# Kernel optimization log

Hardware: AMD Instinct MI355X
Metric: run time of the kernel (lower is better)

## Reference

```python
import jax, jax.numpy as jnp
import numpy as np

# dims (match init_kwargs)
B, S, HID = 2, 2048, 2048
NH = 16
DN = 128   # qk_nope_head_dim
DR = 64    # qk_rope_head_dim
DV = 128   # v_head_dim
QLR = 1536 # q_lora_rank
KVLR = 512 # kv_lora_rank
QHD = DN + DR  # 192
ROPE_BASE = 10000.0
EPS = 1e-6


def rms_norm(x, w):
    # ZeroCenteredRMSNorm: weight is zero-centered, scale = (1 + w)
    var = jnp.mean(x * x, axis=-1, keepdims=True)
    return x * jax.lax.rsqrt(var + EPS) * (1.0 + w)


def rotate_half(x):
    d = x.shape[-1] // 2
    return jnp.concatenate([-x[..., d:], x[..., :d]], axis=-1)


def deinterleave(x):
    # rearrange '(d_pairs two) -> (two d_pairs)'
    return jnp.concatenate([x[..., 0::2], x[..., 1::2]], axis=-1)


def setup_inputs() -> dict:
    key = jax.random.key(0)
    ks = jax.random.split(key, 8)
    s = 0.02
    return {
        "hidden_states": jax.random.normal(ks[0], (B, S, HID), jnp.float32),
        "position_ids": jnp.arange(S, dtype=jnp.int32),
        "Wq_down": jax.random.normal(ks[1], (HID, QLR), jnp.float32) * s,
        "q_norm_w": jnp.zeros((QLR,), jnp.float32),
        "Wq_up": jax.random.normal(ks[2], (QLR, NH * QHD), jnp.float32) * s,
        "Wkv_down": jax.random.normal(ks[3], (HID, KVLR + DR), jnp.float32) * s,
        "kv_norm_w": jnp.zeros((KVLR,), jnp.float32),
        "Wkv_up": jax.random.normal(ks[4], (KVLR, NH * (DN + DV)), jnp.float32) * s,
        "W_gate": jax.random.normal(ks[5], (HID, NH * DV), jnp.float32) * s,
        "W_out": jax.random.normal(ks[6], (NH * DV, HID), jnp.float32) * s,
    }


def reference(hidden_states, position_ids, Wq_down, q_norm_w, Wq_up,
              Wkv_down, kv_norm_w, Wkv_up, W_gate, W_out):
    bsz, q_len, _ = hidden_states.shape
    pos = jnp.broadcast_to(position_ids[None, :], (bsz, q_len))  # [b,s]

    # Q path: down-proj -> RMSNorm -> up-proj -> [b,h,s,QHD]
    q = rms_norm(hidden_states @ Wq_down, q_norm_w) @ Wq_up
    q = q.reshape(bsz, q_len, NH, QHD).transpose(0, 2, 1, 3)
    q_nope, q_rope = q[..., :DN], q[..., DN:]

    # KV path: joint down-proj -> split latent / rope key
    ckv = hidden_states @ Wkv_down                     # [b,s,KVLR+DR]
    c_kv, k_rope = ckv[..., :KVLR], ckv[..., KVLR:]
    k_rope = k_rope[:, None, :, :]                     # [b,1,s,DR]
    kv = rms_norm(c_kv, kv_norm_w) @ Wkv_up            # [b,s,NH*(DN+DV)]
    kv = kv.reshape(bsz, q_len, NH, DN + DV).transpose(0, 2, 1, 3)
    k_nope, v = kv[..., :DN], kv[..., DN:]

    # partial RoPE on rope dims (with the '(pairs two)->(two pairs)' permute)
    inv_freq = 1.0 / (ROPE_BASE ** (jnp.arange(0, DR, 2, dtype=jnp.float32) / DR))
    freqs = pos[..., None].astype(jnp.float32) * inv_freq  # [b,s,DR/2]
    emb = jnp.concatenate([freqs, freqs], axis=-1)          # [b,s,DR]
    cos = jnp.cos(emb)[:, None, :, :]                       # [b,1,s,DR]
    sin = jnp.sin(emb)[:, None, :, :]
    q_r = deinterleave(q_rope)
    k_r = deinterleave(k_rope)
    q_r = q_r * cos + rotate_half(q_r) * sin
    k_r = k_r * cos + rotate_half(k_r) * sin

    query = jnp.concatenate([q_nope, q_r], axis=-1)                       # [b,h,s,QHD]
    key = jnp.concatenate([k_nope, jnp.broadcast_to(k_r, k_nope.shape[:-1] + (DR,))], axis=-1)

    scores = jnp.einsum('bhqd,bhkd->bhqk', query, key) / np.sqrt(QHD)
    attn = jax.nn.softmax(scores, axis=-1)
    out = jnp.einsum('bhqk,bhkd->bhqd', attn, v)                          # [b,h,s,DV]
    out = out.transpose(0, 2, 1, 3)                                       # [b,s,h,DV]

    gate = jax.nn.sigmoid(hidden_states @ W_gate).reshape(bsz, q_len, NH, DV)
    out = (out * gate).reshape(bsz, q_len, NH * DV)
    return out @ W_out
```

## Files before the change

kernel.cpp:

```cpp
#include <hip/hip_runtime.h>
#include <math.h>

#define BT 2
#define SL 2048
#define HIDN 2048
#define NHEADS 16
#define DNOPE 128
#define DROPE 64
#define DVAL 128
#define QHEAD 192
#define QLRANK 1536
#define KVLRANK 512
#define TTOK (BT * SL)

typedef unsigned short u16;
typedef u16 u16x4 __attribute__((ext_vector_type(4)));
typedef u16 u16x8 __attribute__((ext_vector_type(8)));
typedef short bf16x8 __attribute__((ext_vector_type(8)));
typedef float f32x4 __attribute__((ext_vector_type(4)));

__device__ __forceinline__ u16 f2b(float f) {
    union { float f; unsigned u; } v; v.f = f;
    unsigned r = v.u + 0x7FFFu + ((v.u >> 16) & 1u);
    return (u16)(r >> 16);
}
__device__ __forceinline__ float b2f(u16 h) {
    union { unsigned u; float f; } v; v.u = ((unsigned)h) << 16;
    return v.f;
}

__device__ __forceinline__ void gl2lds16(const u16* g, u16* l) {
    __builtin_amdgcn_global_load_lds((const __attribute__((address_space(1))) unsigned int*)g,
                                     (__attribute__((address_space(3))) unsigned int*)l, 16, 0, 0);
}

__global__ __launch_bounds__(256) void cast_k(const float* __restrict__ in, u16* __restrict__ out,
                                              int n4) {
    int i = blockIdx.x * 256 + threadIdx.x;
    const int stride = gridDim.x * 256;
    for (; i < n4; i += stride) {
        const float4 v = ((const float4*)in)[i];
        u16x4 u;
        u.x = f2b(v.x); u.y = f2b(v.y); u.z = f2b(v.z); u.w = f2b(v.w);
        ((u16x4*)out)[i] = u;
    }
}

__global__ __launch_bounds__(256) void tcast_k(const float* __restrict__ in, u16* __restrict__ out,
                                               int R, int C) {
    __shared__ u16 tile[64][72];
    const int c0 = blockIdx.x * 64, r0 = blockIdx.y * 64;
    const int t = threadIdx.x;
    const int tr = t >> 4, tc4 = (t & 15) * 4;
#pragma unroll
    for (int i = 0; i < 4; ++i) {
        const int r = tr + i * 16;
        const float4 v = *(const float4*)&in[(r0 + r) * C + c0 + tc4];
        u16x4 u;
        u.x = f2b(v.x); u.y = f2b(v.y); u.z = f2b(v.z); u.w = f2b(v.w);
        *(u16x4*)&tile[r][tc4] = u;
    }
    __syncthreads();
#pragma unroll
    for (int i = 0; i < 4; ++i) {
        const int rr = tr + i * 16;
        u16x4 u;
        u.x = tile[tc4 + 0][rr];
        u.y = tile[tc4 + 1][rr];
        u.z = tile[tc4 + 2][rr];
        u.w = tile[tc4 + 3][rr];
        *(u16x4*)&out[(c0 + rr) * R + r0 + tc4] = u;
    }
}

__global__ __launch_bounds__(256) void vtrans_k(const u16* __restrict__ kvbuf,
                                                u16* __restrict__ vT) {
    __shared__ u16 tile[64][72];
    const int bh = blockIdx.z;
    const int b = bh >> 4, h = bh & 15;
    const int s0 = blockIdx.x * 64, d0 = blockIdx.y * 64;
    const int t = threadIdx.x;
    const int tr = t >> 4, tc4 = (t & 15) * 4;
#pragma unroll
    for (int i = 0; i < 4; ++i) {
        const int s = tr + i * 16;
        *(u16x4*)&tile[s][tc4] =
            *(const u16x4*)&kvbuf[(b * SL + s0 + s) * 4096 + h * 256 + 128 + d0 + tc4];
    }
    __syncthreads();
#pragma unroll
    for (int i = 0; i < 4; ++i) {
        const int dd = tr + i * 16;
        u16x4 u;
        u.x = tile[tc4 + 0][dd];
        u.y = tile[tc4 + 1][dd];
        u.z = tile[tc4 + 2][dd];
        u.w = tile[tc4 + 3][dd];
        *(u16x4*)&vT[(bh * 128 + d0 + dd) * SL + s0 + tc4] = u;
    }
}

template <int EPI, int OUTF>
__global__ __launch_bounds__(256) void gemm_bf16_k(const u16* __restrict__ A,
                                                   const u16* __restrict__ Bt,
                                                   void* __restrict__ Cv, int M, int N, int K) {
    __shared__ u16 As[128 * 64];
    __shared__ u16 Bs[128 * 64];
    const int t = threadIdx.x;
    const int nx = gridDim.x;
    const int bid = blockIdx.x + nx * blockIdx.y;
    const int cpx = (nx * gridDim.y) >> 3;
    const int swz = (bid & 7) * cpx + (bid >> 3);
    const int bn = (swz % nx) * 128, bm = (swz / nx) * 128;
    const int w = t >> 6, lane = t & 63;
    const int wr = (w >> 1) * 64, wc = (w & 1) * 64;
    const int lr = lane & 15, lg = lane >> 4;

    const int srow = w * 32 + (lane >> 3);
    const int scol = ((lane & 7) ^ ((lane >> 3) & 7)) * 8;
    const u16* Ag = A + (size_t)(bm + srow) * K + scol;
    const u16* Bg = Bt + (size_t)(bn + srow) * K + scol;
    u16* Asl = As + w * 2048;
    u16* Bsl = Bs + w * 2048;

    f32x4 acc[4][4];
#pragma unroll
    for (int i = 0; i < 4; ++i)
#pragma unroll
        for (int j = 0; j < 4; ++j) acc[i][j] = 0.f;

    for (int k0 = 0; k0 < K; k0 += 64) {
        __syncthreads();
#pragma unroll
        for (int j = 0; j < 4; ++j) gl2lds16(Ag + (size_t)(j * 8) * K + k0, Asl + j * 512);
#pragma unroll
        for (int j = 0; j < 4; ++j) gl2lds16(Bg + (size_t)(j * 8) * K + k0, Bsl + j * 512);
        __syncthreads();
#pragma unroll
        for (int kk = 0; kk < 2; ++kk) {
            bf16x8 af[4], bfr[4];
#pragma unroll
            for (int mi = 0; mi < 4; ++mi) {
                const int row = wr + mi * 16 + lr;
                const int idx = (row * 64 + kk * 32 + lg * 8) ^ ((row & 7) << 3);
                af[mi] = *(const bf16x8*)&As[idx];
            }
#pragma unroll
            for (int ni = 0; ni < 4; ++ni) {
                const int row = wc + ni * 16 + lr;
                const int idx = (row * 64 + kk * 32 + lg * 8) ^ ((row & 7) << 3);
                bfr[ni] = *(const bf16x8*)&Bs[idx];
            }
#pragma unroll
            for (int mi = 0; mi < 4; ++mi)
#pragma unroll
                for (int ni = 0; ni < 4; ++ni)
                    acc[mi][ni] = __builtin_amdgcn_mfma_f32_16x16x32_bf16(af[mi], bfr[ni],
                                                                          acc[mi][ni], 0, 0, 0);
        }
    }
#pragma unroll
    for (int mi = 0; mi < 4; ++mi)
#pragma unroll
        for (int ni = 0; ni < 4; ++ni)
#pragma unroll
            for (int r = 0; r < 4; ++r) {
                const int row = bm + wr + mi * 16 + lg * 4 + r;
                const int col = bn + wc + ni * 16 + lr;
                float v = acc[mi][ni][r];
                if (EPI == 1) v = 1.f / (1.f + __expf(-v));
                if (col < N) {
                    if (OUTF)
                        ((float*)Cv)[(size_t)row * N + col] = v;
                    else
                        ((u16*)Cv)[(size_t)row * N + col] = f2b(v);
                }
            }
}

__global__ __launch_bounds__(256) void rmsnorm_k(const u16* __restrict__ in, u16* __restrict__ out,
                                                 const float* __restrict__ w, int is, int os,
                                                 int n) {
    const int row = blockIdx.x;
    const int t = threadIdx.x;
    const u16* x = in + row * is;
    u16* y = out + row * os;
    float ss = 0.f;
    for (int d = t * 4; d < n; d += 1024) {
        const u16x4 u = *(const u16x4*)&x[d];
        const float a = b2f(u.x), b = b2f(u.y), c = b2f(u.z), e = b2f(u.w);
        ss += a * a + b * b + c * c + e * e;
    }
    ss += __shfl_down(ss, 32);
    ss += __shfl_down(ss, 16);
    ss += __shfl_down(ss, 8);
    ss += __shfl_down(ss, 4);
    ss += __shfl_down(ss, 2);
    ss += __shfl_down(ss, 1);
    __shared__ float red[5];
    if ((t & 63) == 0) red[t >> 6] = ss;
    __syncthreads();
    if (t == 0) red[4] = rsqrtf((red[0] + red[1] + red[2] + red[3]) / (float)n + 1e-6f);
    __syncthreads();
    const float sc = red[4];
    for (int d = t * 4; d < n; d += 1024) {
        const u16x4 u = *(const u16x4*)&x[d];
        const float4 wv = *(const float4*)&w[d];
        u16x4 o;
        o.x = f2b(b2f(u.x) * sc * (1.f + wv.x));
        o.y = f2b(b2f(u.y) * sc * (1.f + wv.y));
        o.z = f2b(b2f(u.z) * sc * (1.f + wv.z));
        o.w = f2b(b2f(u.w) * sc * (1.f + wv.w));
        *(u16x4*)&y[d] = o;
    }
}

__global__ __launch_bounds__(64) void rope_k(u16* __restrict__ q, const u16* __restrict__ ckv,
                                             u16* __restrict__ kr, const int* __restrict__ pos_ids) {
    const int tok = blockIdx.x * 2 + (threadIdx.x >> 5);
    const int j = threadIdx.x & 31;
    const int s = tok & (SL - 1);
    const float pos = (float)pos_ids[s];
    const float inv = 1.f / powf(10000.f, (float)(2 * j) / 64.f);
    const float f = pos * inv;
    const float c = cosf(f), sn = sinf(f);
    const u16* kc = ckv + tok * 576 + 512;
    const unsigned kp = *(const unsigned*)&kc[2 * j];
    const float ke = b2f((u16)(kp & 0xffff)), ko = b2f((u16)(kp >> 16));
    kr[tok * 64 + j] = f2b(ke * c - ko * sn);
    kr[tok * 64 + 32 + j] = f2b(ko * c + ke * sn);
#pragma unroll
    for (int h = 0; h < NHEADS; ++h) {
        u16* qb = q + tok * (NHEADS * QHEAD) + h * QHEAD + DNOPE;
        const unsigned qp = *(const unsigned*)&qb[2 * j];
        const float qe = b2f((u16)(qp & 0xffff)), qo = b2f((u16)(qp >> 16));
        qb[j] = f2b(qe * c - qo * sn);
        qb[32 + j] = f2b(qo * c + qe * sn);
    }
}

#define PSTR 76
__global__ __launch_bounds__(256, 2) void mla_attn_k(const u16* __restrict__ qbuf,
                                                     const u16* __restrict__ kvbuf,
                                                     const u16* __restrict__ kr,
                                                     const u16* __restrict__ vT,
                                                     const u16* __restrict__ gateb,
                                                     u16* __restrict__ outg) {
    __shared__ u16 Ks[64 * 200];
    __shared__ u16 Vt[128 * 72];
    __shared__ u16 Ps[4 * 32 * PSTR];
    const int bh = blockIdx.x;
    const int b = bh >> 4, h = bh & 15;
    const int q0 = blockIdx.y * 128;
    const int t = threadIdx.x, w = t >> 6, lane = t & 63;
    const int lr = lane & 15, lg = lane >> 4;
    const float scale = 0.07216878364870322f;

    int kRow[6], kC8[6];
#pragma unroll
    for (int c = 0; c < 6; ++c) {
        const int i = t + c * 256;
        kRow[c] = i / 24;
        kC8[c] = (i % 24) * 8;
    }
    int vRow[4], vC8[4];
#pragma unroll
    for (int c = 0; c < 4; ++c) {
        const int i = t + c * 256;
        vRow[c] = i >> 3;
        vC8[c] = (i & 7) * 8;
    }

    bf16x8 aq[2][6];
#pragma unroll
    for (int mi = 0; mi < 2; ++mi) {
        const int qrow = b * SL + q0 + w * 32 + mi * 16 + lr;
#pragma unroll
        for (int ks = 0; ks < 6; ++ks)
            aq[mi][ks] =
                *(const bf16x8*)&qbuf[(size_t)qrow * (NHEADS * QHEAD) + h * QHEAD + ks * 32 + lg * 8];
    }

    f32x4 O[2][8];
#pragma unroll
    for (int mi = 0; mi < 2; ++mi)
#pragma unroll
        for (int df = 0; df < 8; ++df) O[mi][df] = 0.f;
    float m[2][4], l[2][4];
#pragma unroll
    for (int mi = 0; mi < 2; ++mi)
#pragma unroll
        for (int r = 0; r < 4; ++r) {
            m[mi][r] = -INFINITY;
            l[mi][r] = 0.f;
        }

    u16x8 kreg[6], vreg[4];
#define ATTN_ISSUE_K(K0)                                                                     \
    {                                                                                        \
        _Pragma("unroll") for (int c = 0; c < 6; ++c) {                                      \
            const int tok = b * SL + (K0) + kRow[c];                                         \
            kreg[c] = (kC8[c] < 128)                                                         \
                          ? *(const u16x8*)&kvbuf[(size_t)tok * 4096 + h * 256 + kC8[c]]     \
                          : *(const u16x8*)&kr[(size_t)tok * 64 + (kC8[c] - 128)];           \
        }                                                                                    \
    }
#define ATTN_ISSUE_V(K0)                                                                     \
    {                                                                                        \
        _Pragma("unroll") for (int c = 0; c < 4; ++c)                                        \
            vreg[c] = *(const u16x8*)&vT[(size_t)(bh * 128 + vRow[c]) * SL + (K0) + vC8[c]]; \
    }

    ATTN_ISSUE_K(0);
    ATTN_ISSUE_V(0);

    for (int it = 0; it < SL / 64; ++it) {
        __syncthreads();
#pragma unroll
        for (int c = 0; c < 6; ++c) *(u16x8*)&Ks[kRow[c] * 200 + kC8[c]] = kreg[c];
#pragma unroll
        for (int c = 0; c < 4; ++c) *(u16x8*)&Vt[vRow[c] * 72 + vC8[c]] = vreg[c];
        __syncthreads();
        const bool more = (it + 1) < SL / 64;
        const int kn = (it + 1) * 64;
        if (more) ATTN_ISSUE_K(kn);

        f32x4 s[2][4];
#pragma unroll
        for (int mi = 0; mi < 2; ++mi)
#pragma unroll
            for (int nf = 0; nf < 4; ++nf) s[mi][nf] = 0.f;
#pragma unroll
        for (int ks = 0; ks < 6; ++ks) {
#pragma unroll
            for (int nf = 0; nf < 4; ++nf) {
                const bf16x8 bk = *(const bf16x8*)&Ks[(nf * 16 + lr) * 200 + ks * 32 + lg * 8];
                s[0][nf] = __builtin_amdgcn_mfma_f32_16x16x32_bf16(aq[0][ks], bk, s[0][nf], 0, 0, 0);
                s[1][nf] = __builtin_amdgcn_mfma_f32_16x16x32_bf16(aq[1][ks], bk, s[1][nf], 0, 0, 0);
            }
        }

        float lmv[2][4];
        float growth = -INFINITY;
#pragma unroll
        for (int mi = 0; mi < 2; ++mi)
#pragma unroll
            for (int r = 0; r < 4; ++r) {
                float lm = fmaxf(fmaxf(s[mi][0][r], s[mi][1][r]), fmaxf(s[mi][2][r], s[mi][3][r])) * scale;
                lm = fmaxf(lm, __shfl_xor(lm, 1));
                lm = fmaxf(lm, __shfl_xor(lm, 2));
                lm = fmaxf(lm, __shfl_xor(lm, 4));
                lm = fmaxf(lm, __shfl_xor(lm, 8));
                lmv[mi][r] = lm;
                growth = fmaxf(growth, lm - m[mi][r]);
            }
        const bool skip = __all(growth <= 8.f);

#pragma unroll
        for (int mi = 0; mi < 2; ++mi) {
            const int pb = w * 32 * PSTR + mi * 16 * PSTR;
#pragma unroll
            for (int r = 0; r < 4; ++r) {
                const float mn = skip ? m[mi][r] : fmaxf(m[mi][r], lmv[mi][r]);
                float p0 = __expf(s[mi][0][r] * scale - mn);
                float p1 = __expf(s[mi][1][r] * scale - mn);
                float p2 = __expf(s[mi][2][r] * scale - mn);
                float p3 = __expf(s[mi][3][r] * scale - mn);
                float ps = (p0 + p1) + (p2 + p3);
                ps += __shfl_xor(ps, 1);
                ps += __shfl_xor(ps, 2);
                ps += __shfl_xor(ps, 4);
                ps += __shfl_xor(ps, 8);
                if (skip) {
                    l[mi][r] += ps;
                } else {
                    const float al = __expf(m[mi][r] - mn);
                    l[mi][r] = l[mi][r] * al + ps;
                    m[mi][r] = mn;
#pragma unroll
                    for (int df = 0; df < 8; ++df) O[mi][df][r] *= al;
                }
                const int prow = pb + (lg * 4 + r) * PSTR + lr;
                Ps[prow] = f2b(p0);
                Ps[prow + 16] = f2b(p1);
                Ps[prow + 32] = f2b(p2);
                Ps[prow + 48] = f2b(p3);
            }
        }

        if (more) ATTN_ISSUE_V(kn);

        bf16x8 pa[2][2];
#pragma unroll
        for (int mi = 0; mi < 2; ++mi)
#pragma unroll
            for (int ks2 = 0; ks2 < 2; ++ks2)
                pa[mi][ks2] =
                    *(const bf16x8*)&Ps[w * 32 * PSTR + (mi * 16 + lr) * PSTR + ks2 * 32 + lg * 8];
#pragma unroll
        for (int df = 0; df < 8; ++df)
#pragma unroll
            for (int ks2 = 0; ks2 < 2; ++ks2) {
                const bf16x8 bv = *(const bf16x8*)&Vt[(df * 16 + lr) * 72 + ks2 * 32 + lg * 8];
                O[0][df] = __builtin_amdgcn_mfma_f32_16x16x32_bf16(pa[0][ks2], bv, O[0][df], 0, 0, 0);
                O[1][df] = __builtin_amdgcn_mfma_f32_16x16x32_bf16(pa[1][ks2], bv, O[1][df], 0, 0, 0);
            }
    }
#pragma unroll
    for (int mi = 0; mi < 2; ++mi) {
        float invl[4];
#pragma unroll
        for (int r = 0; r < 4; ++r) invl[r] = 1.f / l[mi][r];
#pragma unroll
        for (int df = 0; df < 8; ++df)
#pragma unroll
            for (int r = 0; r < 4; ++r) {
                const int qq = b * SL + q0 + w * 32 + mi * 16 + lg * 4 + r;
                const int col = h * DVAL + df * 16 + lr;
                const float o = O[mi][df][r] * invl[r];
                const float g = b2f(gateb[qq * (NHEADS * DVAL) + col]);
                outg[qq * (NHEADS * DVAL) + col] = f2b(o * g);
            }
    }
}

extern "C" void kernel_launch(void* const* d_in, const int* in_sizes, int n_in, void* d_out,
                              int out_size, void* d_ws, size_t ws_size, hipStream_t stream) {
    const float* hs = (const float*)d_in[0];
    const int* pos = (const int*)d_in[1];
    const float* Wq_down = (const float*)d_in[2];
    const float* q_norm_w = (const float*)d_in[3];
    const float* Wq_up = (const float*)d_in[4];
    const float* Wkv_down = (const float*)d_in[5];
    const float* kv_norm_w = (const float*)d_in[6];
    const float* Wkv_up = (const float*)d_in[7];
    const float* W_gate = (const float*)d_in[8];
    const float* W_out = (const float*)d_in[9];
    float* out = (float*)d_out;

    u16* p = (u16*)d_ws;
    u16* hs16 = p;      p += (size_t)TTOK * HIDN;
    u16* wqd_t = p;     p += (size_t)QLRANK * HIDN;
    u16* wqu_t = p;     p += (size_t)(NHEADS * QHEAD) * QLRANK;
    u16* wkvd_t = p;    p += (size_t)576 * HIDN;
    u16* wkvu_t = p;    p += (size_t)(NHEADS * 256) * KVLRANK;
    u16* wg_t = p;      p += (size_t)HIDN * HIDN;
    u16* wo_t = p;      p += (size_t)HIDN * (NHEADS * DVAL);
    u16* qdown = p;     p += (size_t)TTOK * QLRANK;
    u16* qbuf = p;      p += (size_t)TTOK * (NHEADS * QHEAD);
    u16* ckv = p;       p += (size_t)TTOK * 576;
    u16* kvn = p;       p += (size_t)TTOK * KVLRANK;
    u16* kvbuf = p;     p += (size_t)TTOK * (NHEADS * 256);
    u16* krb = p;       p += (size_t)TTOK * DROPE;
    u16* vTg = p;       p += (size_t)32 * 128 * SL;
    u16* gateb = p;     p += (size_t)TTOK * (NHEADS * DVAL);
    u16* outg = p;      p += (size_t)TTOK * (NHEADS * DVAL);

    const dim3 blk(256);

    cast_k<<<dim3(2048), blk, 0, stream>>>(hs, hs16, TTOK * HIDN / 4);
    tcast_k<<<dim3(QLRANK / 64, HIDN / 64), blk, 0, stream>>>(Wq_down, wqd_t, HIDN, QLRANK);
    tcast_k<<<dim3((NHEADS * QHEAD) / 64, QLRANK / 64), blk, 0, stream>>>(Wq_up, wqu_t, QLRANK,
                                                                          NHEADS * QHEAD);
    tcast_k<<<dim3(576 / 64, HIDN / 64), blk, 0, stream>>>(Wkv_down, wkvd_t, HIDN, 576);
    tcast_k<<<dim3((NHEADS * 256) / 64, KVLRANK / 64), blk, 0, stream>>>(Wkv_up, wkvu_t, KVLRANK,
                                                                         NHEADS * 256);
    tcast_k<<<dim3(HIDN / 64, HIDN / 64), blk, 0, stream>>>(W_gate, wg_t, HIDN, HIDN);
    tcast_k<<<dim3(HIDN / 64, (NHEADS * DVAL) / 64), blk, 0, stream>>>(W_out, wo_t, NHEADS * DVAL,
                                                                       HIDN);

    gemm_bf16_k<0, 0><<<dim3(QLRANK / 128, TTOK / 128), blk, 0, stream>>>(hs16, wqd_t, qdown, TTOK,
                                                                          QLRANK, HIDN);
    rmsnorm_k<<<dim3(TTOK), blk, 0, stream>>>(qdown, qdown, q_norm_w, QLRANK, QLRANK, QLRANK);
    gemm_bf16_k<0, 0><<<dim3((NHEADS * QHEAD) / 128, TTOK / 128), blk, 0, stream>>>(
        qdown, wqu_t, qbuf, TTOK, NHEADS * QHEAD, QLRANK);
    gemm_bf16_k<0, 0><<<dim3((576 + 127) / 128, TTOK / 128), blk, 0, stream>>>(hs16, wkvd_t, ckv,
                                                                               TTOK, 576, HIDN);
    rmsnorm_k<<<dim3(TTOK), blk, 0, stream>>>(ckv, kvn, kv_norm_w, 576, KVLRANK, KVLRANK);
    gemm_bf16_k<0, 0><<<dim3((NHEADS * 256) / 128, TTOK / 128), blk, 0, stream>>>(
        kvn, wkvu_t, kvbuf, TTOK, NHEADS * 256, KVLRANK);
    rope_k<<<dim3(TTOK / 2), dim3(64), 0, stream>>>(qbuf, ckv, krb, pos);
    vtrans_k<<<dim3(SL / 64, 2, 32), blk, 0, stream>>>(kvbuf, vTg);
    gemm_bf16_k<1, 0><<<dim3((NHEADS * DVAL) / 128, TTOK / 128), blk, 0, stream>>>(
        hs16, wg_t, gateb, TTOK, NHEADS * DVAL, HIDN);

    mla_attn_k<<<dim3(32, SL / 128), blk, 0, stream>>>(qbuf, kvbuf, krb, vTg, gateb, outg);

    gemm_bf16_k<0, 1><<<dim3(HIDN / 128, TTOK / 128), blk, 0, stream>>>(outg, wo_t, out, TTOK, HIDN,
                                                                        NHEADS * DVAL);
}
```

Measured before the change: 497.8 us.

## Fuse q-down, kv-down and gate projections into one wide GEMM

The three GEMMs that all read the bf16 hidden states (q down-projection, kv down-projection and the gate projection) become a single GEMM. It uses a concatenated transposed weight of width 4224 and applies the sigmoid epilogue only to the gate columns. The six weight transpose-cast launches are merged into one kernel, and the two RMSNorm launches into one. RoPE and attention now read their slices of the fused output buffer. This removes repeated reads of the activations, several kernel launches and the poorly-filled 576-wide GEMM. In exchange it computes 64 unused padding columns and uses a wider strided output layout.

```diff
diff --git a/kernel.cpp b/kernel.cpp
--- a/kernel.cpp
+++ b/kernel.cpp
@@ -12,6 +12,10 @@
 #define QLRANK 1536
 #define KVLRANK 512
 #define TTOK (BT * SL)
+#define FN 4224
+#define FC_CKV 1536
+#define FC_ROPE 2048
+#define FC_GATE 2176
 
 typedef unsigned short u16;
 typedef u16 u16x4 __attribute__((ext_vector_type(4)));
@@ -46,16 +50,15 @@
     }
 }
 
-__global__ __launch_bounds__(256) void tcast_k(const float* __restrict__ in, u16* __restrict__ out,
-                                               int R, int C) {
+__device__ __forceinline__ void tcast_tile(const float* __restrict__ in, u16* __restrict__ out,
+                                           int R, int C, int tx, int ty, int t) {
     __shared__ u16 tile[64][72];
-    const int c0 = blockIdx.x * 64, r0 = blockIdx.y * 64;
-    const int t = threadIdx.x;
+    const int c0 = tx * 64, r0 = ty * 64;
     const int tr = t >> 4, tc4 = (t & 15) * 4;
 #pragma unroll
     for (int i = 0; i < 4; ++i) {
         const int r = tr + i * 16;
-        const float4 v = *(const float4*)&in[(r0 + r) * C + c0 + tc4];
+        const float4 v = *(const float4*)&in[(size_t)(r0 + r) * C + c0 + tc4];
         u16x4 u;
         u.x = f2b(v.x); u.y = f2b(v.y); u.z = f2b(v.z); u.w = f2b(v.w);
         *(u16x4*)&tile[r][tc4] = u;
@@ -69,7 +72,35 @@
         u.y = tile[tc4 + 1][rr];
         u.z = tile[tc4 + 2][rr];
         u.w = tile[tc4 + 3][rr];
-        *(u16x4*)&out[(c0 + rr) * R + r0 + tc4] = u;
+        *(u16x4*)&out[(size_t)(c0 + rr) * R + r0 + tc4] = u;
+    }
+}
+
+__global__ __launch_bounds__(256) void tcast_all_k(
+    const float* __restrict__ Wq_down, const float* __restrict__ Wq_up,
+    const float* __restrict__ Wkv_down, const float* __restrict__ Wkv_up,
+    const float* __restrict__ W_gate, const float* __restrict__ W_out, u16* __restrict__ wqd_t,
+    u16* __restrict__ wqu_t, u16* __restrict__ wkvd_t, u16* __restrict__ wkvu_t,
+    u16* __restrict__ wg_t, u16* __restrict__ wo_t) {
+    const int tid = blockIdx.x;
+    const int t = threadIdx.x;
+    if (tid < 768) {
+        tcast_tile(Wq_down, wqd_t, 2048, 1536, tid % 24, tid / 24, t);
+    } else if (tid < 1920) {
+        const int i = tid - 768;
+        tcast_tile(Wq_up, wqu_t, 1536, 3072, i % 48, i / 48, t);
+    } else if (tid < 2208) {
+        const int i = tid - 1920;
+        tcast_tile(Wkv_down, wkvd_t, 2048, 576, i % 9, i / 9, t);
+    } else if (tid < 2720) {
+        const int i = tid - 2208;
+        tcast_tile(Wkv_up, wkvu_t, 512, 4096, i % 64, i / 64, t);
+    } else if (tid < 3744) {
+        const int i = tid - 2720;
+        tcast_tile(W_gate, wg_t, 2048, 2048, i % 32, i / 32, t);
+    } else {
+        const int i = tid - 3744;
+        tcast_tile(W_out, wo_t, 2048, 2048, i % 32, i / 32, t);
     }
 }
 
@@ -85,7 +116,7 @@
     for (int i = 0; i < 4; ++i) {
         const int s = tr + i * 16;
         *(u16x4*)&tile[s][tc4] =
-            *(const u16x4*)&kvbuf[(b * SL + s0 + s) * 4096 + h * 256 + 128 + d0 + tc4];
+            *(const u16x4*)&kvbuf[(size_t)(b * SL + s0 + s) * 4096 + h * 256 + 128 + d0 + tc4];
     }
     __syncthreads();
 #pragma unroll
@@ -96,7 +127,7 @@
         u.y = tile[tc4 + 1][dd];
         u.z = tile[tc4 + 2][dd];
         u.w = tile[tc4 + 3][dd];
-        *(u16x4*)&vT[(bh * 128 + d0 + dd) * SL + s0 + tc4] = u;
+        *(u16x4*)&vT[(size_t)(bh * 128 + d0 + dd) * SL + s0 + tc4] = u;
     }
 }
 
@@ -169,6 +200,7 @@
                 const int col = bn + wc + ni * 16 + lr;
                 float v = acc[mi][ni][r];
                 if (EPI == 1) v = 1.f / (1.f + __expf(-v));
+                if (EPI == 2 && col >= FC_GATE) v = 1.f / (1.f + __expf(-v));
                 if (col < N) {
                     if (OUTF)
                         ((float*)Cv)[(size_t)row * N + col] = v;
@@ -178,13 +210,18 @@
             }
 }
 
-__global__ __launch_bounds__(256) void rmsnorm_k(const u16* __restrict__ in, u16* __restrict__ out,
-                                                 const float* __restrict__ w, int is, int os,
-                                                 int n) {
-    const int row = blockIdx.x;
+__global__ __launch_bounds__(256) void rms2_k(const u16* __restrict__ fout,
+                                              const float* __restrict__ qw,
+                                              const float* __restrict__ kw, u16* __restrict__ qn,
+                                              u16* __restrict__ kvn) {
+    const int rid = blockIdx.x;
+    const bool isq = rid < TTOK;
+    const int row = isq ? rid : rid - TTOK;
+    const int n = isq ? QLRANK : KVLRANK;
+    const u16* x = fout + (size_t)row * FN + (isq ? 0 : FC_CKV);
+    const float* w = isq ? qw : kw;
+    u16* y = isq ? (qn + (size_t)row * QLRANK) : (kvn + (size_t)row * KVLRANK);
     const int t = threadIdx.x;
-    const u16* x = in + row * is;
-    u16* y = out + row * os;
     float ss = 0.f;
     for (int d = t * 4; d < n; d += 1024) {
         const u16x4 u = *(const u16x4*)&x[d];
@@ -215,7 +252,7 @@
     }
 }
 
-__global__ __launch_bounds__(64) void rope_k(u16* __restrict__ q, const u16* __restrict__ ckv,
+__global__ __launch_bounds__(64) void rope_k(u16* __restrict__ q, const u16* __restrict__ fout,
                                              u16* __restrict__ kr, const int* __restrict__ pos_ids) {
     const int tok = blockIdx.x * 2 + (threadIdx.x >> 5);
     const int j = threadIdx.x & 31;
@@ -224,14 +261,14 @@
     const float inv = 1.f / powf(10000.f, (float)(2 * j) / 64.f);
     const float f = pos * inv;
     const float c = cosf(f), sn = sinf(f);
-    const u16* kc = ckv + tok * 576 + 512;
+    const u16* kc = fout + (size_t)tok * FN + FC_ROPE;
     const unsigned kp = *(const unsigned*)&kc[2 * j];
     const float ke = b2f((u16)(kp & 0xffff)), ko = b2f((u16)(kp >> 16));
     kr[tok * 64 + j] = f2b(ke * c - ko * sn);
     kr[tok * 64 + 32 + j] = f2b(ko * c + ke * sn);
 #pragma unroll
     for (int h = 0; h < NHEADS; ++h) {
-        u16* qb = q + tok * (NHEADS * QHEAD) + h * QHEAD + DNOPE;
+        u16* qb = q + (size_t)tok * (NHEADS * QHEAD) + h * QHEAD + DNOPE;
         const unsigned qp = *(const unsigned*)&qb[2 * j];
         const float qe = b2f((u16)(qp & 0xffff)), qo = b2f((u16)(qp >> 16));
         qb[j] = f2b(qe * c - qo * sn);
@@ -418,8 +455,8 @@
                 const int qq = b * SL + q0 + w * 32 + mi * 16 + lg * 4 + r;
                 const int col = h * DVAL + df * 16 + lr;
                 const float o = O[mi][df][r] * invl[r];
-                const float g = b2f(gateb[qq * (NHEADS * DVAL) + col]);
-                outg[qq * (NHEADS * DVAL) + col] = f2b(o * g);
+                const float g = b2f(gateb[(size_t)qq * FN + col]);
+                outg[(size_t)qq * (NHEADS * DVAL) + col] = f2b(o * g);
             }
     }
 }
@@ -440,51 +477,39 @@
 
     u16* p = (u16*)d_ws;
     u16* hs16 = p;      p += (size_t)TTOK * HIDN;
-    u16* wqd_t = p;     p += (size_t)QLRANK * HIDN;
+    u16* wdown_t = p;   p += (size_t)FN * HIDN;
+    u16* wqd_t = wdown_t;
+    u16* wkvd_t = wdown_t + (size_t)QLRANK * HIDN;
+    u16* wg_t = wdown_t + (size_t)FC_GATE * HIDN;
     u16* wqu_t = p;     p += (size_t)(NHEADS * QHEAD) * QLRANK;
-    u16* wkvd_t = p;    p += (size_t)576 * HIDN;
     u16* wkvu_t = p;    p += (size_t)(NHEADS * 256) * KVLRANK;
-    u16* wg_t = p;      p += (size_t)HIDN * HIDN;
     u16* wo_t = p;      p += (size_t)HIDN * (NHEADS * DVAL);
-    u16* qdown = p;     p += (size_t)TTOK * QLRANK;
+    u16* fout = p;      p += (size_t)TTOK * FN;
+    u16* qdownN = p;    p += (size_t)TTOK * QLRANK;
     u16* qbuf = p;      p += (size_t)TTOK * (NHEADS * QHEAD);
-    u16* ckv = p;       p += (size_t)TTOK * 576;
     u16* kvn = p;       p += (size_t)TTOK * KVLRANK;
     u16* kvbuf = p;     p += (size_t)TTOK * (NHEADS * 256);
     u16* krb = p;       p += (size_t)TTOK * DROPE;
     u16* vTg = p;       p += (size_t)32 * 128 * SL;
-    u16* gateb = p;     p += (size_t)TTOK * (NHEADS * DVAL);
     u16* outg = p;      p += (size_t)TTOK * (NHEADS * DVAL);
 
     const dim3 blk(256);
 
     cast_k<<<dim3(2048), blk, 0, stream>>>(hs, hs16, TTOK * HIDN / 4);
-    tcast_k<<<dim3(QLRANK / 64, HIDN / 64), blk, 0, stream>>>(Wq_down, wqd_t, HIDN, QLRANK);
-    tcast_k<<<dim3((NHEADS * QHEAD) / 64, QLRANK / 64), blk, 0, stream>>>(Wq_up, wqu_t, QLRANK,
-                                                                          NHEADS * QHEAD);
-    tcast_k<<<dim3(576 / 64, HIDN / 64), blk, 0, stream>>>(Wkv_down, wkvd_t, HIDN, 576);
-    tcast_k<<<dim3((NHEADS * 256) / 64, KVLRANK / 64), blk, 0, stream>>>(Wkv_up, wkvu_t, KVLRANK,
-                                                                         NHEADS * 256);
-    tcast_k<<<dim3(HIDN / 64, HIDN / 64), blk, 0, stream>>>(W_gate, wg_t, HIDN, HIDN);
-    tcast_k<<<dim3(HIDN / 64, (NHEADS * DVAL) / 64), blk, 0, stream>>>(W_out, wo_t, NHEADS * DVAL,
-                                                                       HIDN);
-
-    gemm_bf16_k<0, 0><<<dim3(QLRANK / 128, TTOK / 128), blk, 0, stream>>>(hs16, wqd_t, qdown, TTOK,
-                                                                          QLRANK, HIDN);
-    rmsnorm_k<<<dim3(TTOK), blk, 0, stream>>>(qdown, qdown, q_norm_w, QLRANK, QLRANK, QLRANK);
+    tcast_all_k<<<dim3(4768), blk, 0, stream>>>(Wq_down, Wq_up, Wkv_down, Wkv_up, W_gate, W_out,
+                                                wqd_t, wqu_t, wkvd_t, wkvu_t, wg_t, wo_t);
+
+    gemm_bf16_k<2, 0><<<dim3(FN / 128, TTOK / 128), blk, 0, stream>>>(hs16, wdown_t, fout, TTOK,
+                                                                      FN, HIDN);
+    rms2_k<<<dim3(2 * TTOK), blk, 0, stream>>>(fout, q_norm_w, kv_norm_w, qdownN, kvn);
     gemm_bf16_k<0, 0><<<dim3((NHEADS * QHEAD) / 128, TTOK / 128), blk, 0, stream>>>(
-        qdown, wqu_t, qbuf, TTOK, NHEADS * QHEAD, QLRANK);
-    gemm_bf16_k<0, 0><<<dim3((576 + 127) / 128, TTOK / 128), blk, 0, stream>>>(hs16, wkvd_t, ckv,
-                                                                               TTOK, 576, HIDN);
-    rmsnorm_k<<<dim3(TTOK), blk, 0, stream>>>(ckv, kvn, kv_norm_w, 576, KVLRANK, KVLRANK);
+        qdownN, wqu_t, qbuf, TTOK, NHEADS * QHEAD, QLRANK);
     gemm_bf16_k<0, 0><<<dim3((NHEADS * 256) / 128, TTOK / 128), blk, 0, stream>>>(
         kvn, wkvu_t, kvbuf, TTOK, NHEADS * 256, KVLRANK);
-    rope_k<<<dim3(TTOK / 2), dim3(64), 0, stream>>>(qbuf, ckv, krb, pos);
+    rope_k<<<dim3(TTOK / 2), dim3(64), 0, stream>>>(qbuf, fout, krb, pos);
     vtrans_k<<<dim3(SL / 64, 2, 32), blk, 0, stream>>>(kvbuf, vTg);
-    gemm_bf16_k<1, 0><<<dim3((NHEADS * DVAL) / 128, TTOK / 128), blk, 0, stream>>>(
-        hs16, wg_t, gateb, TTOK, NHEADS * DVAL, HIDN);
-
-    mla_attn_k<<<dim3(32, SL / 128), blk, 0, stream>>>(qbuf, kvbuf, krb, vTg, gateb, outg);
+
+    mla_attn_k<<<dim3(32, SL / 128), blk, 0, stream>>>(qbuf, kvbuf, krb, vTg, fout + FC_GATE, outg);
 
     gemm_bf16_k<0, 1><<<dim3(HIDN / 128, TTOK / 128), blk, 0, stream>>>(outg, wo_t, out, TTOK, HIDN,
                                                                         NHEADS * DVAL);
```

After: 482.0 us. 1.03x faster.
